# Performance work log

Hardware: AMD Instinct MI355X
Metric: run time of the kernel (lower is better)

Reference implementation:

```python
import jax, jax.numpy as jnp
import numpy as np
from jax import lax


def _gru_layer(x_seq, W, U, b, units):
    """Keras GRU (reset_after=True, gate order [z, r, h]) with activation=relu.
    x_seq: (B, T, F). Returns (ys (B,T,units), h_last (B,units))."""
    b_in, b_rec = b[0], b[1]                      # each (3*units,)
    # Precompute all input projections once: (B, T, 3*units)
    x_proj = jnp.einsum('btf,fj->btj', x_seq, W) + b_in
    B = x_seq.shape[0]
    h0 = jnp.zeros((B, units), dtype=x_seq.dtype)

    def step(h, xp_t):
        rec = h @ U + b_rec                        # (B, 3*units)
        zr = jax.nn.sigmoid(xp_t[:, :2 * units] + rec[:, :2 * units])
        z, r = zr[:, :units], zr[:, units:]
        hh = jax.nn.relu(xp_t[:, 2 * units:] + r * rec[:, 2 * units:])
        h_new = z * h + (1.0 - z) * hh
        return h_new, h_new

    h_last, ys = lax.scan(step, h0, jnp.swapaxes(x_proj, 0, 1))  # scan over T
    return jnp.swapaxes(ys, 0, 1), h_last


def setup_inputs() -> dict:
    key = jax.random.key(0)
    ks = jax.random.split(key, 6)
    B, T, F, U1, U2 = 64, 2048, 15, 256, 256
    s = lambda fan_in: 1.0 / np.sqrt(fan_in)
    return {
        'input_data': jax.random.normal(ks[0], (B, T, F), dtype=jnp.float32),
        'W1': jax.random.normal(ks[1], (F, 3 * U1), dtype=jnp.float32) * s(F),
        'U1': jax.random.normal(ks[2], (U1, 3 * U1), dtype=jnp.float32) * s(U1),
        'b1': jnp.zeros((2, 3 * U1), dtype=jnp.float32),
        'W2': jax.random.normal(ks[3], (U1, 3 * U2), dtype=jnp.float32) * s(U1),
        'U2': jax.random.normal(ks[4], (U2, 3 * U2), dtype=jnp.float32) * s(U2),
        'b2': jnp.zeros((2, 3 * U2), dtype=jnp.float32),
    }


def reference(input_data, W1, U1, b1, W2, U2, b2):
    u1 = U1.shape[0]
    u2 = U2.shape[0]
    seq1, state1 = _gru_layer(input_data, W1, U1, b1, u1)  # gru1: return_sequences + state
    seq2, state2 = _gru_layer(seq1, W2, U2, b2, u2)        # gru2: last output + state
    x = seq2[:, -1, :]                                      # last output (== state2)
    return (x, state1, state2)
```

## Files before the change

### kernel.cpp

```cpp
#include <hip/hip_runtime.h>

#define BB 64
#define TT 2048
#define FF 15
#define UU 256
#define N3 768

typedef _Float16 half8 __attribute__((ext_vector_type(8)));
typedef float f32x4 __attribute__((ext_vector_type(4)));

__device__ _Float16 g_seq1[BB * TT * UU];
__device__ float g_xp[(size_t)BB * TT * N3];
__device__ uint4 g_U1p[48 * 8 * 64];
__device__ uint4 g_U2p[48 * 8 * 64];
__device__ uint4 g_W2p[48 * 8 * 64];

__global__ __launch_bounds__(256) void prep_upk(const float* __restrict__ U,
                                                unsigned* __restrict__ Up) {
    int idx = blockIdx.x * 256 + threadIdx.x;
    int d = idx & 3, l = (idx >> 2) & 63, kt = (idx >> 8) & 7, nt = idx >> 11;
    int row = kt * 32 + ((l >> 4) << 3) + 2 * d;
    int col = nt * 16 + (l & 15);
    unsigned short lo = __builtin_bit_cast(unsigned short, (_Float16)U[row * N3 + col]);
    unsigned short hi = __builtin_bit_cast(unsigned short, (_Float16)U[(row + 1) * N3 + col]);
    Up[idx] = (unsigned)lo | ((unsigned)hi << 16);
}

__global__ __launch_bounds__(256) void gemm_k15(
    const float* __restrict__ x, const float* __restrict__ W1,
    const float* __restrict__ bin, float* __restrict__ C) {
    __shared__ float xr[8][FF];
    const int m0 = blockIdx.x * 8;
    const int j  = blockIdx.y * 256 + threadIdx.x;
    if (threadIdx.x < 8 * FF) {
        int r = threadIdx.x / FF, k = threadIdx.x - r * FF;
        xr[r][k] = x[(size_t)(m0 + r) * FF + k];
    }
    __syncthreads();
    float wv[FF];
#pragma unroll
    for (int k = 0; k < FF; k++) wv[k] = W1[k * N3 + j];
    const float bj = bin[j];
#pragma unroll
    for (int r = 0; r < 8; r++) {
        float a = bj;
#pragma unroll
        for (int k = 0; k < FF; k++) a += xr[r][k] * wv[k];
        C[(size_t)(m0 + r) * N3 + j] = a;
    }
}

__global__ __launch_bounds__(512) void gemm_xp_mfma(
    const _Float16* __restrict__ A, const uint4* __restrict__ Wp,
    const float* __restrict__ bin, float* __restrict__ C) {
    const int tid = threadIdx.x, w = tid >> 6, lane = tid & 63;
    const int mt = w >> 1;
    const int nb = (w & 1) * 24;
    const int arow = blockIdx.x * 64 + mt * 16 + (lane & 15);
    const int ko   = (lane >> 4) * 8;

    f32x4 acc[24] = {};
    const _Float16* ap = A + (size_t)arow * 256 + ko;

#pragma unroll
    for (int kt = 0; kt < 8; kt++) {
        half8 av = *(const half8*)(ap + kt * 32);
        const uint4* wp = Wp + (size_t)(nb * 8 + kt) * 64 + lane;
#pragma unroll
        for (int n = 0; n < 24; n++) {
            half8 bf = __builtin_bit_cast(half8, wp[(size_t)n * 8 * 64]);
            acc[n] = __builtin_amdgcn_mfma_f32_16x16x32_f16(av, bf, acc[n], 0, 0, 0);
        }
    }
    const int rbase = blockIdx.x * 64 + mt * 16 + (lane >> 4) * 4;
#pragma unroll
    for (int n = 0; n < 24; n++) {
        int col = (nb + n) * 16 + (lane & 15);
        float bv = bin[col];
#pragma unroll
        for (int d = 0; d < 4; d++)
            C[(size_t)(rbase + d) * N3 + col] = acc[n][d] + bv;
    }
}

__global__ __launch_bounds__(512) __attribute__((amdgpu_waves_per_eu(2, 2)))
void gru_mfma2(const uint4* __restrict__ Up, const float* __restrict__ brec,
               const float* __restrict__ xp, _Float16* __restrict__ seq_out,
               float* __restrict__ state_out, float* __restrict__ extra_out) {
    const int b = blockIdx.x, tid = threadIdx.x;
    const int w = tid >> 6, lane = tid & 63;
    const int l15 = lane & 15;
    const int uA = 32 * w + l15, uB = uA + 16;

    __shared__ __align__(16) _Float16 h2s[2][UU];

    const int tz = 2 * w, tr = 16 + 2 * w, th = 32 + 2 * w;
    half8 ub[48];
#pragma unroll
    for (int kt = 0; kt < 8; kt++) {
        ub[0 * 8 + kt] = __builtin_bit_cast(half8, Up[((tz + 0) * 8 + kt) * 64 + lane]);
        ub[1 * 8 + kt] = __builtin_bit_cast(half8, Up[((tz + 1) * 8 + kt) * 64 + lane]);
        ub[2 * 8 + kt] = __builtin_bit_cast(half8, Up[((tr + 0) * 8 + kt) * 64 + lane]);
        ub[3 * 8 + kt] = __builtin_bit_cast(half8, Up[((tr + 1) * 8 + kt) * 64 + lane]);
        ub[4 * 8 + kt] = __builtin_bit_cast(half8, Up[((th + 0) * 8 + kt) * 64 + lane]);
        ub[5 * 8 + kt] = __builtin_bit_cast(half8, Up[((th + 1) * 8 + kt) * 64 + lane]);
    }
    const float brzA = brec[uA], brrA = brec[uA + UU], brhA = brec[uA + 2 * UU];
    const float brzB = brec[uB], brrB = brec[uB + UU], brhB = brec[uB + 2 * UU];

    if (tid < 128) ((unsigned*)h2s[0])[tid] = 0u;
    float hA = 0.f, hB = 0.f;
    __syncthreads();

    const float* __restrict__ xpb = xp + (size_t)b * TT * N3;
    float xzA = xpb[uA], xrA = xpb[uA + UU], xhA = xpb[uA + 2 * UU];
    float xzB = xpb[uB], xrB = xpb[uB + UU], xhB = xpb[uB + 2 * UU];

    const int arow = (lane >> 4) << 3;

    for (int t = 0; t < TT; t++) {
        const float* xn = xpb + (size_t)(t + 1 < TT ? t + 1 : t) * N3;
        float xzAn = xn[uA], xrAn = xn[uA + UU], xhAn = xn[uA + 2 * UU];
        float xzBn = xn[uB], xrBn = xn[uB + UU], xhBn = xn[uB + 2 * UU];

        const _Float16* hcur = h2s[t & 1];
        f32x4 a0 = {0.f, 0.f, 0.f, 0.f}, a1 = a0, a2 = a0, a3 = a0, a4 = a0, a5 = a0;
#pragma unroll
        for (int kt = 0; kt < 8; kt++) {
            half8 av = *(const half8*)&hcur[kt * 32 + arow];
            a0 = __builtin_amdgcn_mfma_f32_16x16x32_f16(av, ub[0 * 8 + kt], a0, 0, 0, 0);
            a1 = __builtin_amdgcn_mfma_f32_16x16x32_f16(av, ub[1 * 8 + kt], a1, 0, 0, 0);
            a2 = __builtin_amdgcn_mfma_f32_16x16x32_f16(av, ub[2 * 8 + kt], a2, 0, 0, 0);
            a3 = __builtin_amdgcn_mfma_f32_16x16x32_f16(av, ub[3 * 8 + kt], a3, 0, 0, 0);
            a4 = __builtin_amdgcn_mfma_f32_16x16x32_f16(av, ub[4 * 8 + kt], a4, 0, 0, 0);
            a5 = __builtin_amdgcn_mfma_f32_16x16x32_f16(av, ub[5 * 8 + kt], a5, 0, 0, 0);
        }

        float zA = 1.f / (1.f + __expf(-(xzA + a0[0] + brzA)));
        float zB = 1.f / (1.f + __expf(-(xzB + a1[0] + brzB)));
        float rA = 1.f / (1.f + __expf(-(xrA + a2[0] + brrA)));
        float rB = 1.f / (1.f + __expf(-(xrB + a3[0] + brrB)));
        float hhA = xhA + rA * (a4[0] + brhA); hhA = hhA > 0.f ? hhA : 0.f;
        float hhB = xhB + rB * (a5[0] + brhB); hhB = hhB > 0.f ? hhB : 0.f;
        hA = zA * hA + (1.f - zA) * hhA;
        hB = zB * hB + (1.f - zB) * hhB;

        _Float16* hnxt = h2s[(t + 1) & 1];
        if (lane < 32) {
            int   u  = (lane < 16) ? uA : uB;
            float hv = (lane < 16) ? hA : hB;
            _Float16 hq = (_Float16)hv;
            hnxt[u] = hq;
            if (seq_out)
                seq_out[(size_t)b * TT * UU + (size_t)t * UU + u] = hq;
        }
        __syncthreads();
        xzA = xzAn; xrA = xrAn; xhA = xhAn;
        xzB = xzBn; xrB = xrBn; xhB = xhBn;
    }

    if (lane < 32) {
        int   u  = (lane < 16) ? uA : uB;
        float hv = (lane < 16) ? hA : hB;
        state_out[b * UU + u] = hv;
        if (extra_out) extra_out[b * UU + u] = hv;
    }
}

extern "C" void kernel_launch(void* const* d_in, const int* in_sizes, int n_in,
                              void* d_out, int out_size, void* d_ws, size_t ws_size,
                              hipStream_t stream) {
    const float* x  = (const float*)d_in[0];
    const float* W1 = (const float*)d_in[1];
    const float* U1 = (const float*)d_in[2];
    const float* b1 = (const float*)d_in[3];
    const float* W2 = (const float*)d_in[4];
    const float* U2 = (const float*)d_in[5];
    const float* b2 = (const float*)d_in[6];
    float* out = (float*)d_out;

    uint4* U1p; hipGetSymbolAddress((void**)&U1p, HIP_SYMBOL(g_U1p));
    uint4* U2p; hipGetSymbolAddress((void**)&U2p, HIP_SYMBOL(g_U2p));
    uint4* W2p; hipGetSymbolAddress((void**)&W2p, HIP_SYMBOL(g_W2p));
    _Float16* seq1; hipGetSymbolAddress((void**)&seq1, HIP_SYMBOL(g_seq1));
    float* xp;      hipGetSymbolAddress((void**)&xp,   HIP_SYMBOL(g_xp));

    prep_upk<<<384, 256, 0, stream>>>(U1, (unsigned*)U1p);
    prep_upk<<<384, 256, 0, stream>>>(U2, (unsigned*)U2p);
    prep_upk<<<384, 256, 0, stream>>>(W2, (unsigned*)W2p);

    gemm_k15<<<dim3(BB * TT / 8, 3), 256, 0, stream>>>(x, W1, b1, xp);
    gru_mfma2<<<BB, 512, 0, stream>>>(U1p, b1 + N3, xp, seq1, out + BB * UU, nullptr);

    gemm_xp_mfma<<<BB * TT / 64, 512, 0, stream>>>(seq1, W2p, b2, xp);
    gru_mfma2<<<BB, 512, 0, stream>>>(U2p, b2 + N3, xp, nullptr, out + 2 * BB * UU, out);
}
```

Measured before the change: 4.959 ms.

## Split GRU recurrence across 16 waves and fold recurrent z/r bias into input projection

```diff
diff --git a/kernel.cpp b/kernel.cpp
--- a/kernel.cpp
+++ b/kernel.cpp
@@ -28,7 +28,8 @@
 
 __global__ __launch_bounds__(256) void gemm_k15(
     const float* __restrict__ x, const float* __restrict__ W1,
-    const float* __restrict__ bin, float* __restrict__ C) {
+    const float* __restrict__ bin, const float* __restrict__ brec,
+    float* __restrict__ C) {
     __shared__ float xr[8][FF];
     const int m0 = blockIdx.x * 8;
     const int j  = blockIdx.y * 256 + threadIdx.x;
@@ -40,7 +41,7 @@
     float wv[FF];
 #pragma unroll
     for (int k = 0; k < FF; k++) wv[k] = W1[k * N3 + j];
-    const float bj = bin[j];
+    const float bj = bin[j] + (j < 2 * UU ? brec[j] : 0.f);
 #pragma unroll
     for (int r = 0; r < 8; r++) {
         float a = bj;
@@ -52,7 +53,8 @@
 
 __global__ __launch_bounds__(512) void gemm_xp_mfma(
     const _Float16* __restrict__ A, const uint4* __restrict__ Wp,
-    const float* __restrict__ bin, float* __restrict__ C) {
+    const float* __restrict__ bin, const float* __restrict__ brec,
+    float* __restrict__ C) {
     const int tid = threadIdx.x, w = tid >> 6, lane = tid & 63;
     const int mt = w >> 1;
     const int nb = (w & 1) * 24;
@@ -76,94 +78,76 @@
 #pragma unroll
     for (int n = 0; n < 24; n++) {
         int col = (nb + n) * 16 + (lane & 15);
-        float bv = bin[col];
+        float bv = bin[col] + (col < 2 * UU ? brec[col] : 0.f);
 #pragma unroll
         for (int d = 0; d < 4; d++)
             C[(size_t)(rbase + d) * N3 + col] = acc[n][d] + bv;
     }
 }
 
-__global__ __launch_bounds__(512) __attribute__((amdgpu_waves_per_eu(2, 2)))
-void gru_mfma2(const uint4* __restrict__ Up, const float* __restrict__ brec,
-               const float* __restrict__ xp, _Float16* __restrict__ seq_out,
-               float* __restrict__ state_out, float* __restrict__ extra_out) {
+__global__ __launch_bounds__(1024) __attribute__((amdgpu_waves_per_eu(4, 4)))
+void gru_mfma16(const uint4* __restrict__ Up, const float* __restrict__ brec,
+                const float* __restrict__ xp, _Float16* __restrict__ seq_out,
+                float* __restrict__ state_out, float* __restrict__ extra_out) {
     const int b = blockIdx.x, tid = threadIdx.x;
     const int w = tid >> 6, lane = tid & 63;
     const int l15 = lane & 15;
-    const int uA = 32 * w + l15, uB = uA + 16;
+    const int uA = 16 * w + l15;
 
     __shared__ __align__(16) _Float16 h2s[2][UU];
 
-    const int tz = 2 * w, tr = 16 + 2 * w, th = 32 + 2 * w;
-    half8 ub[48];
+    half8 ub[24];
 #pragma unroll
     for (int kt = 0; kt < 8; kt++) {
-        ub[0 * 8 + kt] = __builtin_bit_cast(half8, Up[((tz + 0) * 8 + kt) * 64 + lane]);
-        ub[1 * 8 + kt] = __builtin_bit_cast(half8, Up[((tz + 1) * 8 + kt) * 64 + lane]);
-        ub[2 * 8 + kt] = __builtin_bit_cast(half8, Up[((tr + 0) * 8 + kt) * 64 + lane]);
-        ub[3 * 8 + kt] = __builtin_bit_cast(half8, Up[((tr + 1) * 8 + kt) * 64 + lane]);
-        ub[4 * 8 + kt] = __builtin_bit_cast(half8, Up[((th + 0) * 8 + kt) * 64 + lane]);
-        ub[5 * 8 + kt] = __builtin_bit_cast(half8, Up[((th + 1) * 8 + kt) * 64 + lane]);
+        ub[0 * 8 + kt] = __builtin_bit_cast(half8, Up[((w)      * 8 + kt) * 64 + lane]);
+        ub[1 * 8 + kt] = __builtin_bit_cast(half8, Up[((16 + w) * 8 + kt) * 64 + lane]);
+        ub[2 * 8 + kt] = __builtin_bit_cast(half8, Up[((32 + w) * 8 + kt) * 64 + lane]);
     }
-    const float brzA = brec[uA], brrA = brec[uA + UU], brhA = brec[uA + 2 * UU];
-    const float brzB = brec[uB], brrB = brec[uB + UU], brhB = brec[uB + 2 * UU];
+    const float brh = brec[uA + 2 * UU];
 
     if (tid < 128) ((unsigned*)h2s[0])[tid] = 0u;
-    float hA = 0.f, hB = 0.f;
+    float h = 0.f;
     __syncthreads();
 
     const float* __restrict__ xpb = xp + (size_t)b * TT * N3;
-    float xzA = xpb[uA], xrA = xpb[uA + UU], xhA = xpb[uA + 2 * UU];
-    float xzB = xpb[uB], xrB = xpb[uB + UU], xhB = xpb[uB + 2 * UU];
+    float xz = xpb[uA], xr = xpb[uA + UU], xh = xpb[uA + 2 * UU];
 
     const int arow = (lane >> 4) << 3;
 
     for (int t = 0; t < TT; t++) {
         const float* xn = xpb + (size_t)(t + 1 < TT ? t + 1 : t) * N3;
-        float xzAn = xn[uA], xrAn = xn[uA + UU], xhAn = xn[uA + 2 * UU];
-        float xzBn = xn[uB], xrBn = xn[uB + UU], xhBn = xn[uB + 2 * UU];
+        float xzn = xn[uA], xrn = xn[uA + UU], xhn = xn[uA + 2 * UU];
 
         const _Float16* hcur = h2s[t & 1];
-        f32x4 a0 = {0.f, 0.f, 0.f, 0.f}, a1 = a0, a2 = a0, a3 = a0, a4 = a0, a5 = a0;
+        f32x4 a0 = {0.f, 0.f, 0.f, 0.f}, a1 = a0, a2 = a0;
 #pragma unroll
         for (int kt = 0; kt < 8; kt++) {
             half8 av = *(const half8*)&hcur[kt * 32 + arow];
             a0 = __builtin_amdgcn_mfma_f32_16x16x32_f16(av, ub[0 * 8 + kt], a0, 0, 0, 0);
             a1 = __builtin_amdgcn_mfma_f32_16x16x32_f16(av, ub[1 * 8 + kt], a1, 0, 0, 0);
             a2 = __builtin_amdgcn_mfma_f32_16x16x32_f16(av, ub[2 * 8 + kt], a2, 0, 0, 0);
-            a3 = __builtin_amdgcn_mfma_f32_16x16x32_f16(av, ub[3 * 8 + kt], a3, 0, 0, 0);
-            a4 = __builtin_amdgcn_mfma_f32_16x16x32_f16(av, ub[4 * 8 + kt], a4, 0, 0, 0);
-            a5 = __builtin_amdgcn_mfma_f32_16x16x32_f16(av, ub[5 * 8 + kt], a5, 0, 0, 0);
         }
 
-        float zA = 1.f / (1.f + __expf(-(xzA + a0[0] + brzA)));
-        float zB = 1.f / (1.f + __expf(-(xzB + a1[0] + brzB)));
-        float rA = 1.f / (1.f + __expf(-(xrA + a2[0] + brrA)));
-        float rB = 1.f / (1.f + __expf(-(xrB + a3[0] + brrB)));
-        float hhA = xhA + rA * (a4[0] + brhA); hhA = hhA > 0.f ? hhA : 0.f;
-        float hhB = xhB + rB * (a5[0] + brhB); hhB = hhB > 0.f ? hhB : 0.f;
-        hA = zA * hA + (1.f - zA) * hhA;
-        hB = zB * hB + (1.f - zB) * hhB;
+        float z  = 1.f / (1.f + __expf(-(xz + a0[0])));
+        float r  = 1.f / (1.f + __expf(-(xr + a1[0])));
+        float hh = xh + r * (a2[0] + brh);
+        hh = hh > 0.f ? hh : 0.f;
+        h = z * h + (1.f - z) * hh;
 
         _Float16* hnxt = h2s[(t + 1) & 1];
-        if (lane < 32) {
-            int   u  = (lane < 16) ? uA : uB;
-            float hv = (lane < 16) ? hA : hB;
-            _Float16 hq = (_Float16)hv;
-            hnxt[u] = hq;
+        if (lane < 16) {
+            _Float16 hq = (_Float16)h;
+            hnxt[uA] = hq;
             if (seq_out)
-                seq_out[(size_t)b * TT * UU + (size_t)t * UU + u] = hq;
+                seq_out[(size_t)b * TT * UU + (size_t)t * UU + uA] = hq;
         }
         __syncthreads();
-        xzA = xzAn; xrA = xrAn; xhA = xhAn;
-        xzB = xzBn; xrB = xrBn; xhB = xhBn;
+        xz = xzn; xr = xrn; xh = xhn;
     }
 
-    if (lane < 32) {
-        int   u  = (lane < 16) ? uA : uB;
-        float hv = (lane < 16) ? hA : hB;
-        state_out[b * UU + u] = hv;
-        if (extra_out) extra_out[b * UU + u] = hv;
+    if (lane < 16) {
+        state_out[b * UU + uA] = h;
+        if (extra_out) extra_out[b * UU + uA] = h;
     }
 }
 
@@ -189,9 +173,9 @@
     prep_upk<<<384, 256, 0, stream>>>(U2, (unsigned*)U2p);
     prep_upk<<<384, 256, 0, stream>>>(W2, (unsigned*)W2p);
 
-    gemm_k15<<<dim3(BB * TT / 8, 3), 256, 0, stream>>>(x, W1, b1, xp);
-    gru_mfma2<<<BB, 512, 0, stream>>>(U1p, b1 + N3, xp, seq1, out + BB * UU, nullptr);
+    gemm_k15<<<dim3(BB * TT / 8, 3), 256, 0, stream>>>(x, W1, b1, b1 + N3, xp);
+    gru_mfma16<<<BB, 1024, 0, stream>>>(U1p, b1 + N3, xp, seq1, out + BB * UU, nullptr);
 
-    gemm_xp_mfma<<<BB * TT / 64, 512, 0, stream>>>(seq1, W2p, b2, xp);
-    gru_mfma2<<<BB, 512, 0, stream>>>(U2p, b2 + N3, xp, nullptr, out + 2 * BB * UU, out);
+    gemm_xp_mfma<<<BB * TT / 64, 512, 0, stream>>>(seq1, W2p, b2, b2 + N3, xp);
+    gru_mfma16<<<BB, 1024, 0, stream>>>(U2p, b2 + N3, xp, nullptr, out + 2 * BB * UU, out);
 }
```

Measured after the change: 4.492 ms (median of 2 runs). 1.1x faster.
